# Kernel tuning notes

Hardware: AMD Instinct MI355X
Metric: run time of the kernel (lower is better)

Reference implementation:

```python
import jax, jax.numpy as jnp
import numpy as np

N_SPK = 8      # MAX_NO_OF_SPEAKERS
N_LAYERS = 2


def setup_inputs() -> dict:
    key = jax.random.key(0)
    B, S, H = 8, 1024, 512  # batch, seq_len, input_size==hidden_size==output_size
    k = jax.random.split(key, 6)
    x = jax.random.normal(k[0], (B, S, H), dtype=jnp.float32)
    speakers = jax.random.randint(k[1], (B, S), 0, N_SPK, dtype=jnp.int32)
    scale = 1.0 / np.sqrt(H).astype(np.float32)
    # per-speaker, per-layer GRU params (torch nn.GRU layout: gates [r,z,n])
    Wi = jax.random.uniform(k[2], (N_SPK, N_LAYERS, 3 * H, H), minval=-scale, maxval=scale, dtype=jnp.float32)
    Wh = jax.random.uniform(k[3], (N_SPK, N_LAYERS, 3 * H, H), minval=-scale, maxval=scale, dtype=jnp.float32)
    bi = jax.random.uniform(k[4], (N_SPK, N_LAYERS, 3 * H), minval=-scale, maxval=scale, dtype=jnp.float32)
    bh = jax.random.uniform(k[5], (N_SPK, N_LAYERS, 3 * H), minval=-scale, maxval=scale, dtype=jnp.float32)
    return {"x": x, "speakers": speakers, "Wi": Wi, "Wh": Wh, "bi": bi, "bh": bh}


def _gru_cell(x_t, h, Wi_l, Wh_l, bi_l, bh_l):
    # torch GRU cell: r,z,n gates
    gi = x_t @ Wi_l.T + bi_l          # [B, 3H]
    gh = h @ Wh_l.T + bh_l            # [B, 3H]
    ir, iz, i_n = jnp.split(gi, 3, axis=-1)
    hr, hz, h_n = jnp.split(gh, 3, axis=-1)
    r = jax.nn.sigmoid(ir + hr)
    z = jax.nn.sigmoid(iz + hz)
    n = jnp.tanh(i_n + r * h_n)
    return (1.0 - z) * n + z * h


def _forward(x, speakers, Wi, Wh, bi, bh):
    B, S, H = x.shape
    x_sb = jnp.swapaxes(x, 0, 1)              # [S, B, H]
    total = jnp.zeros((S, B, H), x.dtype)
    for sp in range(N_SPK):
        # masked-GRU equivalence: gathering speaker sp's utterances, running a
        # GRU, and scattering back == running over the full sequence while
        # freezing hidden state (and emitting 0) at non-sp timesteps.
        mask_sb = (speakers == sp).T          # [S, B]
        Wi_s, Wh_s, bi_s, bh_s = Wi[sp], Wh[sp], bi[sp], bh[sp]

        def step(h, xm):
            x_t, m_t = xm                     # [B,H], [B]
            m = m_t[:, None]
            inp = x_t
            new_h = []
            for l in range(N_LAYERS):
                hl = _gru_cell(inp, h[l], Wi_s[l], Wh_s[l], bi_s[l], bh_s[l])
                hl = jnp.where(m, hl, h[l])   # carry hidden across masked steps
                new_h.append(hl)
                inp = hl
            return jnp.stack(new_h), jnp.where(m, inp, 0.0)

        h0 = jnp.zeros((N_LAYERS, B, H), x.dtype)
        _, outs = jax.lax.scan(step, h0, (x_sb, mask_sb))  # outs: [S, B, H]
        total = total + outs                  # masks disjoint across speakers
    return jnp.swapaxes(total, 0, 1)          # [B, S, H]


def reference(x, speakers, Wi, Wh, bi, bh):
    return _forward(x, speakers, Wi, Wh, bi, bh)
```

## Files before the change

kernel.cpp:

```cpp
#include <hip/hip_runtime.h>
#include <cstdint>
#include <cstddef>

#define SS 1024
#define HH 512
#define G3 1536

typedef _Float16 half8 __attribute__((ext_vector_type(8)));
typedef float f32x4 __attribute__((ext_vector_type(4)));
typedef unsigned u32x4 __attribute__((ext_vector_type(4)));

static constexpr unsigned OFF_TLIST = 0;
static constexpr unsigned OFF_LEN   = 262144;
static constexpr unsigned OFF_META  = 262400;
static constexpr unsigned OFF_H0    = 262656;
static constexpr unsigned OFF_H1    = OFF_H0 + 524288;
static constexpr unsigned OFF_FLG   = OFF_H1 + 524288;
static constexpr unsigned WS_NEED   = OFF_FLG + 4096;

__device__ __forceinline__ half8 cvt8(const float* p) {
  float4 u = *(const float4*)p;
  float4 v = *(const float4*)(p + 4);
  half8 h;
  h[0]=(_Float16)u.x; h[1]=(_Float16)u.y; h[2]=(_Float16)u.z; h[3]=(_Float16)u.w;
  h[4]=(_Float16)v.x; h[5]=(_Float16)v.y; h[6]=(_Float16)v.z; h[7]=(_Float16)v.w;
  return h;
}

__device__ __forceinline__ float sigm(float x) { return 1.f / (1.f + __expf(-x)); }

__device__ __forceinline__ unsigned wavemin64(unsigned v) {
#pragma unroll
  for (int d = 1; d < 64; d <<= 1) {
    unsigned o = (unsigned)__shfl_xor((int)v, d, 64);
    v = (o < v) ? o : v;
  }
  return v;
}

__device__ __forceinline__ void poll1(const unsigned* f, unsigned tgt) {
  const int l = threadIdx.x & 63;
  unsigned it = 0;
  for (;;) {
    unsigned v = __hip_atomic_load(f + l, __ATOMIC_RELAXED, __HIP_MEMORY_SCOPE_AGENT);
    if (__all((int)(v >= tgt))) return;
    if (++it > 64u) __builtin_amdgcn_s_sleep(1);
    if (it > 20000000u) return;
  }
}
__device__ __forceinline__ void poll2(const unsigned* f0, const unsigned* f1, unsigned tgt) {
  const int l = threadIdx.x & 63;
  unsigned it = 0;
  for (;;) {
    unsigned v0 = __hip_atomic_load(f0 + l, __ATOMIC_RELAXED, __HIP_MEMORY_SCOPE_AGENT);
    unsigned v1 = __hip_atomic_load(f1 + l, __ATOMIC_RELAXED, __HIP_MEMORY_SCOPE_AGENT);
    if (__all((int)(v0 >= tgt && v1 >= tgt))) return;
    if (++it > 64u) __builtin_amdgcn_s_sleep(1);
    if (it > 20000000u) return;
  }
}

__device__ __forceinline__ void uc_ld2(const unsigned* p, u32x4& a, u32x4& b) {
  asm volatile(
    "global_load_dwordx4 %0, %2, off sc0 sc1\n\t"
    "global_load_dwordx4 %1, %2, off offset:16 sc0 sc1\n\t"
    "s_waitcnt vmcnt(0)"
    : "=&v"(a), "=&v"(b) : "v"(p) : "memory");
  __builtin_amdgcn_sched_barrier(0);
}
__device__ __forceinline__ void uc_ld4(const unsigned* p, const unsigned* q,
                                       u32x4& a, u32x4& b, u32x4& c, u32x4& d) {
  asm volatile(
    "global_load_dwordx4 %0, %4, off sc0 sc1\n\t"
    "global_load_dwordx4 %1, %4, off offset:16 sc0 sc1\n\t"
    "global_load_dwordx4 %2, %5, off sc0 sc1\n\t"
    "global_load_dwordx4 %3, %5, off offset:16 sc0 sc1\n\t"
    "s_waitcnt vmcnt(0)"
    : "=&v"(a), "=&v"(b), "=&v"(c), "=&v"(d) : "v"(p), "v"(q) : "memory");
  __builtin_amdgcn_sched_barrier(0);
}

__device__ __forceinline__ void uc_st32(unsigned* p, unsigned v) {
  __hip_atomic_store(p, v, __ATOMIC_RELAXED, __HIP_MEMORY_SCOPE_AGENT);
}
__device__ __forceinline__ void uc_st64(unsigned long long* p, unsigned long long v) {
  __hip_atomic_store(p, v, __ATOMIC_RELAXED, __HIP_MEMORY_SCOPE_AGENT);
}

__global__ void prep_kernel(const int* __restrict__ spk, int* __restrict__ tlist,
                            int* __restrict__ len, int* __restrict__ meta) {
  __shared__ int slen[64];
  const int t = threadIdx.x;
  const int sp = t >> 3, b = t & 7;
  int cnt = 0;
  int* tl = tlist + (sp * 8 + b) * SS;
  const int4* srow = (const int4*)(spk + b * SS);
#pragma unroll 4
  for (int i = 0; i < SS / 4; ++i) {
    int4 v = srow[i];
    if (v.x == sp) tl[cnt++] = 4 * i + 0;
    if (v.y == sp) tl[cnt++] = 4 * i + 1;
    if (v.z == sp) tl[cnt++] = 4 * i + 2;
    if (v.w == sp) tl[cnt++] = 4 * i + 3;
  }
  len[t] = cnt;
  slen[t] = cnt;
  for (int i = cnt; i < SS; ++i) tl[i] = 0;
  __syncthreads();
  if (t < 8) {
    int m = 0;
    for (int i = 0; i < 8; ++i) m = max(m, slen[t * 8 + i]);
    meta[t] = m;
  }
}

__launch_bounds__(256, 1)
__global__ void gru_main(const float* __restrict__ x,
                         const float* __restrict__ Wi, const float* __restrict__ Wh,
                         const float* __restrict__ bi, const float* __restrict__ bh,
                         const int* __restrict__ tlist, const int* __restrict__ len,
                         const int* __restrict__ meta,
                         unsigned short* __restrict__ h0ring,
                         unsigned short* __restrict__ h1ring,
                         unsigned* __restrict__ flg, float* __restrict__ out) {
  const int wg = blockIdx.x;
  const int L  = wg & 1;
  const int sp = (wg >> 1) & 7;
  const int og = wg >> 4;
  const int j0 = og * 32;
  const int tid = threadIdx.x;
  const int w  = tid >> 6;
  const int l  = tid & 63;
  const int b8 = l & 7;

  __shared__ __align__(16) _Float16 hstA[8][552];
  __shared__ __align__(16) _Float16 hstB[8][552];
  __shared__ __align__(16) _Float16 xst[2][8][552];
  __shared__ float sc[4][2][8][28];
  __shared__ __align__(8) unsigned short psc[4][64];

  unsigned* flg0 = flg + (0 * 8 + sp) * 64;
  unsigned* flg1 = flg + (1 * 8 + sp) * 64;

  const size_t WMAT = (size_t)G3 * HH;
  const float* pWi = Wi + (size_t)(sp * 2 + L) * WMAT;
  const float* pWh = Wh + (size_t)(sp * 2 + L) * WMAT;
  const int cc0 = l & 15;
  int wrow0, wrow1;
  if (cc0 < 12) {
    wrow0 = (cc0 >> 2) * HH + j0 + 8 * w + 0 + (cc0 & 3);
    wrow1 = (cc0 >> 2) * HH + j0 + 8 * w + 4 + (cc0 & 3);
  } else { wrow0 = 0; wrow1 = 0; }
  half8 bwI0[16], bwI1[16], bwH0[16], bwH1[16];
#pragma unroll
  for (int q = 0; q < 16; ++q) {
    const int k0 = (l >> 4) * 8 + q * 32;
    bwI0[q] = cvt8(pWi + (size_t)wrow0 * HH + k0);
    bwI1[q] = cvt8(pWi + (size_t)wrow1 * HH + k0);
    bwH0[q] = cvt8(pWh + (size_t)wrow0 * HH + k0);
    bwH1[q] = cvt8(pWh + (size_t)wrow1 * HH + k0);
  }

  const int gb = l >> 3, gj = l & 7;
  const int jmy = j0 + 8 * w + gj;
  const int lenG = len[sp * 8 + gb];
  const int* tlG = tlist + (sp * 8 + gb) * SS;
  float bgi[3], bgh[3];
#pragma unroll
  for (int g = 0; g < 3; ++g) {
    bgi[g] = bi[(sp * 2 + L) * G3 + g * HH + jmy];
    bgh[g] = bh[(sp * 2 + L) * G3 + g * HH + jmy];
  }
  const int lenP = len[sp * 8 + ((l >> 1) & 7)];

  const int R = meta[sp];
  float hprev = 0.f;
  unsigned r1min = 0;

  const int t6 = (gj >> 2) * 12, c4 = gj & 3;
  const int cc = l & 15, rg = l >> 4;
  const int stg_b = tid >> 5, stg_k = (tid & 31) * 16;

  if (L == 0) {
    {
      const int tx = tlist[(sp * 8 + stg_b) * SS + 0];
      const float* xs = x + ((size_t)stg_b * SS + tx) * HH + stg_k;
      _Float16* dst = &xst[0][stg_b][stg_k];
      *(half8*)dst = cvt8(xs);
      *(half8*)(dst + 8) = cvt8(xs + 8);
    }

    for (int r = 0; r < R; ++r) {
      if (r > 0) poll1(flg0, (unsigned)r);
      {
        const unsigned* src = (const unsigned*)(h0ring +
            ((size_t)(((r - 1) & 7) * 64 + sp * 8)) * HH) + tid * 8;
        u32x4 a, b;
        uc_ld2(src, a, b);
        u32x4* d = (u32x4*)&hstA[stg_b][stg_k];
        d[0] = a; d[1] = b;
      }
      __syncthreads();

      f32x4 aI0, aI1, aH0, aH1;
#pragma unroll
      for (int e = 0; e < 4; ++e) { aI0[e]=0.f; aI1[e]=0.f; aH0[e]=0.f; aH1[e]=0.f; }
      {
        const _Float16* hrow = &hstA[b8][(l >> 4) * 8];
        const _Float16* xrow = &xst[r & 1][b8][(l >> 4) * 8];
#pragma unroll
        for (int q = 0; q < 16; ++q) {
          half8 ha = *(const half8*)(hrow + q * 32);
          half8 xa = *(const half8*)(xrow + q * 32);
          aH0 = __builtin_amdgcn_mfma_f32_16x16x32_f16(ha, bwH0[q], aH0, 0, 0, 0);
          aH1 = __builtin_amdgcn_mfma_f32_16x16x32_f16(ha, bwH1[q], aH1, 0, 0, 0);
          aI0 = __builtin_amdgcn_mfma_f32_16x16x32_f16(xa, bwI0[q], aI0, 0, 0, 0);
          aI1 = __builtin_amdgcn_mfma_f32_16x16x32_f16(xa, bwI1[q], aI1, 0, 0, 0);
        }
      }

      if (cc < 12 && rg < 2) {
#pragma unroll
        for (int e = 0; e < 4; ++e) {
          sc[w][0][rg * 4 + e][cc]      = aI0[e];
          sc[w][0][rg * 4 + e][12 + cc] = aI1[e];
          sc[w][1][rg * 4 + e][cc]      = aH0[e];
          sc[w][1][rg * 4 + e][12 + cc] = aH1[e];
        }
      }
      asm volatile("s_waitcnt lgkmcnt(0)" ::: "memory");
      __builtin_amdgcn_sched_barrier(0);
      {
        float gi[3], gh[3];
#pragma unroll
        for (int g = 0; g < 3; ++g) {
          gi[g] = sc[w][0][gb][t6 + g * 4 + c4] + bgi[g];
          gh[g] = sc[w][1][gb][t6 + g * 4 + c4] + bgh[g];
        }
        const float rr_ = sigm(gi[0] + gh[0]);
        const float zz  = sigm(gi[1] + gh[1]);
        const float nn  = tanhf(gi[2] + rr_ * gh[2]);
        if (r < lenG) hprev = (1.f - zz) * nn + zz * hprev;
      }
      union { _Float16 hf; unsigned short us; } cv; cv.hf = (_Float16)hprev;
      psc[w][l] = cv.us;
      asm volatile("s_waitcnt lgkmcnt(0)" ::: "memory");
      __builtin_amdgcn_sched_barrier(0);

      if (r >= 7 && (int)r1min < r - 6) {
        unsigned it = 0;
        for (;;) {
          unsigned v = __hip_atomic_load(flg1 + l, __ATOMIC_RELAXED, __HIP_MEMORY_SCOPE_AGENT);
          r1min = wavemin64(v);
          if ((int)r1min >= r - 6) break;
          __builtin_amdgcn_s_sleep(1);
          if (++it > 20000000u) break;
        }
      }

      if (l < 16 && r < lenP) {
        const int pb = l >> 1;
        unsigned long long v = *(const unsigned long long*)&psc[w][(pb << 3) + ((l & 1) << 2)];
        unsigned long long* dst = (unsigned long long*)(h0ring +
            ((size_t)((r & 7) * 64 + sp * 8 + pb)) * HH + j0 + 8 * w + ((l & 1) << 2));
        uc_st64(dst, v);
      }
      asm volatile("s_waitcnt vmcnt(0)" ::: "memory");
      __builtin_amdgcn_sched_barrier(0);
      if (l == 0) uc_st32(&flg0[og * 4 + w], (unsigned)(r + 1));

      {
        const int tx = tlist[(sp * 8 + stg_b) * SS + ((r + 1) & (SS - 1))];
        const float* xs = x + ((size_t)stg_b * SS + tx) * HH + stg_k;
        _Float16* dst = &xst[(r + 1) & 1][stg_b][stg_k];
        *(half8*)dst = cvt8(xs);
        *(half8*)(dst + 8) = cvt8(xs + 8);
      }
      {
        unsigned v = __hip_atomic_load(flg1 + l, __ATOMIC_RELAXED, __HIP_MEMORY_SCOPE_AGENT);
        r1min = wavemin64(v);
      }
    }
  } else {
    for (int r = 0; r <= R; ++r) {
      if (r > 0) poll2(flg0, flg1, (unsigned)r);
      {
        const unsigned* pa = (const unsigned*)(h0ring +
            ((size_t)(((r - 1) & 7) * 64 + sp * 8)) * HH) + tid * 8;
        const unsigned* pb = (const unsigned*)(h1ring +
            ((size_t)(((r - 2) & 7) * 64 + sp * 8)) * HH) + tid * 8;
        u32x4 a, b, c, d2;
        uc_ld4(pa, pb, a, b, c, d2);
        u32x4* da = (u32x4*)&hstA[stg_b][stg_k];
        u32x4* db = (u32x4*)&hstB[stg_b][stg_k];
        da[0] = a; da[1] = b; db[0] = c; db[1] = d2;
      }
      __syncthreads();

      f32x4 aI0, aI1, aH0, aH1;
#pragma unroll
      for (int e = 0; e < 4; ++e) { aI0[e]=0.f; aI1[e]=0.f; aH0[e]=0.f; aH1[e]=0.f; }
      {
        const _Float16* arow = &hstA[b8][(l >> 4) * 8];
        const _Float16* brow = &hstB[b8][(l >> 4) * 8];
#pragma unroll
        for (int q = 0; q < 16; ++q) {
          half8 ha = *(const half8*)(arow + q * 32);
          half8 hb = *(const half8*)(brow + q * 32);
          aI0 = __builtin_amdgcn_mfma_f32_16x16x32_f16(ha, bwI0[q], aI0, 0, 0, 0);
          aI1 = __builtin_amdgcn_mfma_f32_16x16x32_f16(ha, bwI1[q], aI1, 0, 0, 0);
          aH0 = __builtin_amdgcn_mfma_f32_16x16x32_f16(hb, bwH0[q], aH0, 0, 0, 0);
          aH1 = __builtin_amdgcn_mfma_f32_16x16x32_f16(hb, bwH1[q], aH1, 0, 0, 0);
        }
      }

      if (cc < 12 && rg < 2) {
#pragma unroll
        for (int e = 0; e < 4; ++e) {
          sc[w][0][rg * 4 + e][cc]      = aI0[e];
          sc[w][0][rg * 4 + e][12 + cc] = aI1[e];
          sc[w][1][rg * 4 + e][cc]      = aH0[e];
          sc[w][1][rg * 4 + e][12 + cc] = aH1[e];
        }
      }
      asm volatile("s_waitcnt lgkmcnt(0)" ::: "memory");
      __builtin_amdgcn_sched_barrier(0);
      const bool act = (r >= 1) && (r <= lenG);
      {
        float gi[3], gh[3];
#pragma unroll
        for (int g = 0; g < 3; ++g) {
          gi[g] = sc[w][0][gb][t6 + g * 4 + c4] + bgi[g];
          gh[g] = sc[w][1][gb][t6 + g * 4 + c4] + bgh[g];
        }
        const float rr_ = sigm(gi[0] + gh[0]);
        const float zz  = sigm(gi[1] + gh[1]);
        const float nn  = tanhf(gi[2] + rr_ * gh[2]);
        if (act) hprev = (1.f - zz) * nn + zz * hprev;
      }
      union { _Float16 hf; unsigned short us; } cv; cv.hf = (_Float16)hprev;
      psc[w][l] = cv.us;
      asm volatile("s_waitcnt lgkmcnt(0)" ::: "memory");
      __builtin_amdgcn_sched_barrier(0);

      if (l < 16 && r >= 1 && r <= lenP) {
        const int pb = l >> 1;
        unsigned long long v = *(const unsigned long long*)&psc[w][(pb << 3) + ((l & 1) << 2)];
        unsigned long long* dst = (unsigned long long*)(h1ring +
            ((size_t)(((r - 1) & 7) * 64 + sp * 8 + pb)) * HH + j0 + 8 * w + ((l & 1) << 2));
        uc_st64(dst, v);
      }
      asm volatile("s_waitcnt vmcnt(0)" ::: "memory");
      __builtin_amdgcn_sched_barrier(0);
      if (l == 0) uc_st32(&flg1[og * 4 + w], (unsigned)(r + 1));

      if (act) {
        const int tcur = tlG[(r - 1) & (SS - 1)];
        out[((size_t)(gb * SS + tcur)) * HH + jmy] = hprev;
      }
    }
  }
}

extern "C" void kernel_launch(void* const* d_in, const int* in_sizes, int n_in,
                              void* d_out, int out_size, void* d_ws, size_t ws_size,
                              hipStream_t stream) {
  const float* x   = (const float*)d_in[0];
  const int*   spk = (const int*)d_in[1];
  const float* Wi  = (const float*)d_in[2];
  const float* Wh  = (const float*)d_in[3];
  const float* bi  = (const float*)d_in[4];
  const float* bh  = (const float*)d_in[5];
  float* out = (float*)d_out;
  char* ws = (char*)d_ws;

  int*            tlist = (int*)(ws + OFF_TLIST);
  int*            len   = (int*)(ws + OFF_LEN);
  int*            meta  = (int*)(ws + OFF_META);
  unsigned short* h0r   = (unsigned short*)(ws + OFF_H0);
  unsigned short* h1r   = (unsigned short*)(ws + OFF_H1);
  unsigned*       flg   = (unsigned*)(ws + OFF_FLG);

  (void)in_sizes; (void)n_in; (void)out_size; (void)ws_size;

  hipMemsetAsync(ws + OFF_H0, 0, WS_NEED - OFF_H0, stream);
  prep_kernel<<<1, 64, 0, stream>>>(spk, tlist, len, meta);
  gru_main<<<256, 256, 0, stream>>>(x, Wi, Wh, bi, bh, tlist, len, meta,
                                    h0r, h1r, flg, out);
}
```

Before: 721.4 us.

## Replace flag-based handoff with sequence-tagged hidden-state ring entries

Each fp16 hidden value is now stored in a 32-bit word with the step number in the upper half. Consumers poll the data itself and re-read only the chunks whose tags are stale. This removes the separate store-then-wait-then-flag handshake and the consumer's flag poll on the layer-0 to layer-1 critical path. The layer-1 back-pressure flag is now written once per workgroup right after its loads instead of once per wave after its stores. In exchange the ring traffic doubles, and stores are now unconditional for all batch rows, including padded steps.

```diff
diff --git a/kernel.cpp b/kernel.cpp
--- a/kernel.cpp
+++ b/kernel.cpp
@@ -14,8 +14,8 @@
 static constexpr unsigned OFF_LEN   = 262144;
 static constexpr unsigned OFF_META  = 262400;
 static constexpr unsigned OFF_H0    = 262656;
-static constexpr unsigned OFF_H1    = OFF_H0 + 524288;
-static constexpr unsigned OFF_FLG   = OFF_H1 + 524288;
+static constexpr unsigned OFF_H1    = OFF_H0 + 1048576;
+static constexpr unsigned OFF_FLG   = OFF_H1 + 1048576;
 static constexpr unsigned WS_NEED   = OFF_FLG + 4096;
 
 __device__ __forceinline__ half8 cvt8(const float* p) {
@@ -27,7 +27,21 @@
   return h;
 }
 
+__device__ __forceinline__ half8 pack8(u32x4 a, u32x4 b) {
+  union { unsigned u[4]; half8 h; } r;
+  r.u[0] = __builtin_amdgcn_perm(a[1], a[0], 0x05040100);
+  r.u[1] = __builtin_amdgcn_perm(a[3], a[2], 0x05040100);
+  r.u[2] = __builtin_amdgcn_perm(b[1], b[0], 0x05040100);
+  r.u[3] = __builtin_amdgcn_perm(b[3], b[2], 0x05040100);
+  return r.h;
+}
+
 __device__ __forceinline__ float sigm(float x) { return 1.f / (1.f + __expf(-x)); }
+
+__device__ __forceinline__ unsigned tagbad(u32x4 v, unsigned exp) {
+  return ((v[0] >> 16) ^ exp) | ((v[1] >> 16) ^ exp) |
+         ((v[2] >> 16) ^ exp) | ((v[3] >> 16) ^ exp);
+}
 
 __device__ __forceinline__ unsigned wavemin64(unsigned v) {
 #pragma unroll
@@ -38,45 +52,40 @@
   return v;
 }
 
-__device__ __forceinline__ void poll1(const unsigned* f, unsigned tgt) {
-  const int l = threadIdx.x & 63;
-  unsigned it = 0;
-  for (;;) {
-    unsigned v = __hip_atomic_load(f + l, __ATOMIC_RELAXED, __HIP_MEMORY_SCOPE_AGENT);
-    if (__all((int)(v >= tgt))) return;
-    if (++it > 64u) __builtin_amdgcn_s_sleep(1);
-    if (it > 20000000u) return;
-  }
-}
-__device__ __forceinline__ void poll2(const unsigned* f0, const unsigned* f1, unsigned tgt) {
-  const int l = threadIdx.x & 63;
-  unsigned it = 0;
-  for (;;) {
-    unsigned v0 = __hip_atomic_load(f0 + l, __ATOMIC_RELAXED, __HIP_MEMORY_SCOPE_AGENT);
-    unsigned v1 = __hip_atomic_load(f1 + l, __ATOMIC_RELAXED, __HIP_MEMORY_SCOPE_AGENT);
-    if (__all((int)(v0 >= tgt && v1 >= tgt))) return;
-    if (++it > 64u) __builtin_amdgcn_s_sleep(1);
-    if (it > 20000000u) return;
-  }
-}
-
-__device__ __forceinline__ void uc_ld2(const unsigned* p, u32x4& a, u32x4& b) {
-  asm volatile(
-    "global_load_dwordx4 %0, %2, off sc0 sc1\n\t"
-    "global_load_dwordx4 %1, %2, off offset:16 sc0 sc1\n\t"
-    "s_waitcnt vmcnt(0)"
-    : "=&v"(a), "=&v"(b) : "v"(p) : "memory");
+__device__ __forceinline__ u32x4 uc_ld16(const unsigned* p) {
+  u32x4 d;
+  asm volatile("global_load_dwordx4 %0, %1, off sc0 sc1\n\ts_waitcnt vmcnt(0)"
+               : "=v"(d) : "v"(p) : "memory");
   __builtin_amdgcn_sched_barrier(0);
-}
-__device__ __forceinline__ void uc_ld4(const unsigned* p, const unsigned* q,
-                                       u32x4& a, u32x4& b, u32x4& c, u32x4& d) {
+  return d;
+}
+__device__ __forceinline__ void uc_ld4s(const unsigned* p,
+                                        u32x4& a0, u32x4& a1, u32x4& a2, u32x4& a3) {
   asm volatile(
     "global_load_dwordx4 %0, %4, off sc0 sc1\n\t"
     "global_load_dwordx4 %1, %4, off offset:16 sc0 sc1\n\t"
-    "global_load_dwordx4 %2, %5, off sc0 sc1\n\t"
-    "global_load_dwordx4 %3, %5, off offset:16 sc0 sc1\n\t"
+    "global_load_dwordx4 %2, %4, off offset:32 sc0 sc1\n\t"
+    "global_load_dwordx4 %3, %4, off offset:48 sc0 sc1\n\t"
     "s_waitcnt vmcnt(0)"
-    : "=&v"(a), "=&v"(b), "=&v"(c), "=&v"(d) : "v"(p), "v"(q) : "memory");
+    : "=&v"(a0), "=&v"(a1), "=&v"(a2), "=&v"(a3) : "v"(p) : "memory");
+  __builtin_amdgcn_sched_barrier(0);
+}
+__device__ __forceinline__ void uc_ld8d(const unsigned* p, const unsigned* q,
+                                        u32x4& a0, u32x4& a1, u32x4& a2, u32x4& a3,
+                                        u32x4& b0, u32x4& b1, u32x4& b2, u32x4& b3) {
+  asm volatile(
+    "global_load_dwordx4 %0, %8, off sc0 sc1\n\t"
+    "global_load_dwordx4 %1, %8, off offset:16 sc0 sc1\n\t"
+    "global_load_dwordx4 %2, %8, off offset:32 sc0 sc1\n\t"
+    "global_load_dwordx4 %3, %8, off offset:48 sc0 sc1\n\t"
+    "global_load_dwordx4 %4, %9, off sc0 sc1\n\t"
+    "global_load_dwordx4 %5, %9, off offset:16 sc0 sc1\n\t"
+    "global_load_dwordx4 %6, %9, off offset:32 sc0 sc1\n\t"
+    "global_load_dwordx4 %7, %9, off offset:48 sc0 sc1\n\t"
+    "s_waitcnt vmcnt(0)"
+    : "=&v"(a0), "=&v"(a1), "=&v"(a2), "=&v"(a3),
+      "=&v"(b0), "=&v"(b1), "=&v"(b2), "=&v"(b3)
+    : "v"(p), "v"(q) : "memory");
   __builtin_amdgcn_sched_barrier(0);
 }
 
@@ -120,8 +129,7 @@
                          const float* __restrict__ bi, const float* __restrict__ bh,
                          const int* __restrict__ tlist, const int* __restrict__ len,
                          const int* __restrict__ meta,
-                         unsigned short* __restrict__ h0ring,
-                         unsigned short* __restrict__ h1ring,
+                         unsigned* __restrict__ h0ring, unsigned* __restrict__ h1ring,
                          unsigned* __restrict__ flg, float* __restrict__ out) {
   const int wg = blockIdx.x;
   const int L  = wg & 1;
@@ -139,8 +147,7 @@
   __shared__ float sc[4][2][8][28];
   __shared__ __align__(8) unsigned short psc[4][64];
 
-  unsigned* flg0 = flg + (0 * 8 + sp) * 64;
-  unsigned* flg1 = flg + (1 * 8 + sp) * 64;
+  unsigned* flg1 = flg + sp * 16;
 
   const size_t WMAT = (size_t)G3 * HH;
   const float* pWi = Wi + (size_t)(sp * 2 + L) * WMAT;
@@ -171,7 +178,6 @@
     bgi[g] = bi[(sp * 2 + L) * G3 + g * HH + jmy];
     bgh[g] = bh[(sp * 2 + L) * G3 + g * HH + jmy];
   }
-  const int lenP = len[sp * 8 + ((l >> 1) & 7)];
 
   const int R = meta[sp];
   float hprev = 0.f;
@@ -179,7 +185,8 @@
 
   const int t6 = (gj >> 2) * 12, c4 = gj & 3;
   const int cc = l & 15, rg = l >> 4;
-  const int stg_b = tid >> 5, stg_k = (tid & 31) * 16;
+  const int stg_b = tid >> 5;
+  const int stg_k = (tid & 31) * 16;
 
   if (L == 0) {
     {
@@ -191,14 +198,26 @@
     }
 
     for (int r = 0; r < R; ++r) {
-      if (r > 0) poll1(flg0, (unsigned)r);
-      {
-        const unsigned* src = (const unsigned*)(h0ring +
-            ((size_t)(((r - 1) & 7) * 64 + sp * 8)) * HH) + tid * 8;
-        u32x4 a, b;
-        uc_ld2(src, a, b);
-        u32x4* d = (u32x4*)&hstA[stg_b][stg_k];
-        d[0] = a; d[1] = b;
+      {
+        const unsigned exp = (unsigned)r;
+        const unsigned* src = h0ring +
+            ((size_t)(((r - 1) & 7) * 64 + sp * 8)) * HH + tid * 16;
+        u32x4 q0, q1, q2, q3;
+        uc_ld4s(src, q0, q1, q2, q3);
+        unsigned it = 0;
+        for (;;) {
+          const unsigned d0 = tagbad(q0, exp), d1 = tagbad(q1, exp);
+          const unsigned d2 = tagbad(q2, exp), d3 = tagbad(q3, exp);
+          if (!(d0 | d1 | d2 | d3)) break;
+          if (++it > 16u) __builtin_amdgcn_s_sleep(1);
+          if (it > 5000000u) break;
+          if (d0) q0 = uc_ld16(src + 0);
+          if (d1) q1 = uc_ld16(src + 4);
+          if (d2) q2 = uc_ld16(src + 8);
+          if (d3) q3 = uc_ld16(src + 12);
+        }
+        *(half8*)&hstA[stg_b][stg_k]     = pack8(q0, q1);
+        *(half8*)&hstA[stg_b][stg_k + 8] = pack8(q2, q3);
       }
       __syncthreads();
 
@@ -250,24 +269,28 @@
       if (r >= 7 && (int)r1min < r - 6) {
         unsigned it = 0;
         for (;;) {
-          unsigned v = __hip_atomic_load(flg1 + l, __ATOMIC_RELAXED, __HIP_MEMORY_SCOPE_AGENT);
+          unsigned v = __hip_atomic_load(flg1 + (l & 15), __ATOMIC_RELAXED,
+                                         __HIP_MEMORY_SCOPE_AGENT);
           r1min = wavemin64(v);
           if ((int)r1min >= r - 6) break;
           __builtin_amdgcn_s_sleep(1);
-          if (++it > 20000000u) break;
-        }
-      }
-
-      if (l < 16 && r < lenP) {
-        const int pb = l >> 1;
-        unsigned long long v = *(const unsigned long long*)&psc[w][(pb << 3) + ((l & 1) << 2)];
-        unsigned long long* dst = (unsigned long long*)(h0ring +
-            ((size_t)((r & 7) * 64 + sp * 8 + pb)) * HH + j0 + 8 * w + ((l & 1) << 2));
-        uc_st64(dst, v);
-      }
-      asm volatile("s_waitcnt vmcnt(0)" ::: "memory");
-      __builtin_amdgcn_sched_barrier(0);
-      if (l == 0) uc_st32(&flg0[og * 4 + w], (unsigned)(r + 1));
+          if (++it > 5000000u) break;
+        }
+      }
+
+      {
+        const unsigned tagw = ((unsigned)(r + 1)) << 16;
+        if (l < 32) {
+          const int pb = l >> 2, pr = l & 3;
+          const unsigned v = *(const unsigned*)&psc[w][pb * 8 + 2 * pr];
+          const unsigned long long d =
+              (unsigned long long)(tagw | (v & 0xffffu)) |
+              ((unsigned long long)(tagw | (v >> 16)) << 32);
+          unsigned long long* dst = (unsigned long long*)(h0ring +
+              ((size_t)((r & 7) * 64 + sp * 8 + pb)) * HH + j0 + 8 * w + 2 * pr);
+          uc_st64(dst, d);
+        }
+      }
 
       {
         const int tx = tlist[(sp * 8 + stg_b) * SS + ((r + 1) & (SS - 1))];
@@ -277,25 +300,46 @@
         *(half8*)(dst + 8) = cvt8(xs + 8);
       }
       {
-        unsigned v = __hip_atomic_load(flg1 + l, __ATOMIC_RELAXED, __HIP_MEMORY_SCOPE_AGENT);
+        unsigned v = __hip_atomic_load(flg1 + (l & 15), __ATOMIC_RELAXED,
+                                       __HIP_MEMORY_SCOPE_AGENT);
         r1min = wavemin64(v);
       }
     }
   } else {
     for (int r = 0; r <= R; ++r) {
-      if (r > 0) poll2(flg0, flg1, (unsigned)r);
-      {
-        const unsigned* pa = (const unsigned*)(h0ring +
-            ((size_t)(((r - 1) & 7) * 64 + sp * 8)) * HH) + tid * 8;
-        const unsigned* pb = (const unsigned*)(h1ring +
-            ((size_t)(((r - 2) & 7) * 64 + sp * 8)) * HH) + tid * 8;
-        u32x4 a, b, c, d2;
-        uc_ld4(pa, pb, a, b, c, d2);
-        u32x4* da = (u32x4*)&hstA[stg_b][stg_k];
-        u32x4* db = (u32x4*)&hstB[stg_b][stg_k];
-        da[0] = a; da[1] = b; db[0] = c; db[1] = d2;
+      {
+        const unsigned exp = (unsigned)r;
+        const unsigned* pa = h0ring +
+            ((size_t)(((r - 1) & 7) * 64 + sp * 8)) * HH + tid * 16;
+        const unsigned* pb = h1ring +
+            ((size_t)(((r - 2) & 7) * 64 + sp * 8)) * HH + tid * 16;
+        u32x4 a0, a1, a2, a3, c0, c1, c2, c3;
+        uc_ld8d(pa, pb, a0, a1, a2, a3, c0, c1, c2, c3);
+        unsigned it = 0;
+        for (;;) {
+          const unsigned d0 = tagbad(a0, exp), d1 = tagbad(a1, exp);
+          const unsigned d2 = tagbad(a2, exp), d3 = tagbad(a3, exp);
+          const unsigned e0 = tagbad(c0, exp), e1 = tagbad(c1, exp);
+          const unsigned e2 = tagbad(c2, exp), e3 = tagbad(c3, exp);
+          if (!(d0 | d1 | d2 | d3 | e0 | e1 | e2 | e3)) break;
+          if (++it > 16u) __builtin_amdgcn_s_sleep(1);
+          if (it > 5000000u) break;
+          if (d0) a0 = uc_ld16(pa + 0);
+          if (d1) a1 = uc_ld16(pa + 4);
+          if (d2) a2 = uc_ld16(pa + 8);
+          if (d3) a3 = uc_ld16(pa + 12);
+          if (e0) c0 = uc_ld16(pb + 0);
+          if (e1) c1 = uc_ld16(pb + 4);
+          if (e2) c2 = uc_ld16(pb + 8);
+          if (e3) c3 = uc_ld16(pb + 12);
+        }
+        *(half8*)&hstA[stg_b][stg_k]     = pack8(a0, a1);
+        *(half8*)&hstA[stg_b][stg_k + 8] = pack8(a2, a3);
+        *(half8*)&hstB[stg_b][stg_k]     = pack8(c0, c1);
+        *(half8*)&hstB[stg_b][stg_k + 8] = pack8(c2, c3);
       }
       __syncthreads();
+      if (tid == 0) uc_st32(&flg1[og], (unsigned)(r + 1));
 
       f32x4 aI0, aI1, aH0, aH1;
 #pragma unroll
@@ -343,16 +387,19 @@
       asm volatile("s_waitcnt lgkmcnt(0)" ::: "memory");
       __builtin_amdgcn_sched_barrier(0);
 
-      if (l < 16 && r >= 1 && r <= lenP) {
-        const int pb = l >> 1;
-        unsigned long long v = *(const unsigned long long*)&psc[w][(pb << 3) + ((l & 1) << 2)];
-        unsigned long long* dst = (unsigned long long*)(h1ring +
-            ((size_t)(((r - 1) & 7) * 64 + sp * 8 + pb)) * HH + j0 + 8 * w + ((l & 1) << 2));
-        uc_st64(dst, v);
-      }
-      asm volatile("s_waitcnt vmcnt(0)" ::: "memory");
-      __builtin_amdgcn_sched_barrier(0);
-      if (l == 0) uc_st32(&flg1[og * 4 + w], (unsigned)(r + 1));
+      {
+        const unsigned tagw = ((unsigned)(r + 1)) << 16;
+        if (l < 32) {
+          const int pb = l >> 2, pr = l & 3;
+          const unsigned v = *(const unsigned*)&psc[w][pb * 8 + 2 * pr];
+          const unsigned long long d =
+              (unsigned long long)(tagw | (v & 0xffffu)) |
+              ((unsigned long long)(tagw | (v >> 16)) << 32);
+          unsigned long long* dst = (unsigned long long*)(h1ring +
+              ((size_t)(((r - 1) & 7) * 64 + sp * 8 + pb)) * HH + j0 + 8 * w + 2 * pr);
+          uc_st64(dst, d);
+        }
+      }
 
       if (act) {
         const int tcur = tlG[(r - 1) & (SS - 1)];
@@ -374,12 +421,12 @@
   float* out = (float*)d_out;
   char* ws = (char*)d_ws;
 
-  int*            tlist = (int*)(ws + OFF_TLIST);
-  int*            len   = (int*)(ws + OFF_LEN);
-  int*            meta  = (int*)(ws + OFF_META);
-  unsigned short* h0r   = (unsigned short*)(ws + OFF_H0);
-  unsigned short* h1r   = (unsigned short*)(ws + OFF_H1);
-  unsigned*       flg   = (unsigned*)(ws + OFF_FLG);
+  int*      tlist = (int*)(ws + OFF_TLIST);
+  int*      len   = (int*)(ws + OFF_LEN);
+  int*      meta  = (int*)(ws + OFF_META);
+  unsigned* h0r   = (unsigned*)(ws + OFF_H0);
+  unsigned* h1r   = (unsigned*)(ws + OFF_H1);
+  unsigned* flg   = (unsigned*)(ws + OFF_FLG);
 
   (void)in_sizes; (void)n_in; (void)out_size; (void)ws_size;
 
```

Measured after the change: 666.7 us. -7.6%, faster.
